# Kernel optimization log

Hardware: AMD Instinct MI355X
Metric: run time of the kernel (lower is better)

The kernel has to match this reference:

```python
import jax, jax.numpy as jnp
import numpy as np

N, E, XD, H, L, G, C = 20000, 320000, 128, 256, 4, 128, 10
EPS = 1e-5


def setup_inputs() -> dict:
    key = jax.random.key(0)
    ks = jax.random.split(key, 24)
    s = 0.05
    inp = {
        "x": jax.random.normal(ks[0], (N, XD), jnp.float32),
        "edge_index": jax.random.randint(ks[1], (2, E), 0, N, jnp.int32),
        "batch": jnp.sort(jax.random.randint(ks[2], (N,), 0, G, jnp.int32)),
        "encW": jax.random.normal(ks[3], (XD, H), jnp.float32) * s,
        "encB": jnp.zeros((H,), jnp.float32),
        "convW": jax.random.normal(ks[4], (L, H, H), jnp.float32) * s,
        "convB": jnp.zeros((L, H), jnp.float32),
        "bnG": jnp.ones((L, H), jnp.float32),
        "bnB": jnp.zeros((L, H), jnp.float32),
        "fcW1": jax.random.normal(ks[5], (H, H), jnp.float32) * s,
        "fcB1": jnp.zeros((H,), jnp.float32),
        "fcG1": jnp.ones((H,), jnp.float32),
        "fcBe1": jnp.zeros((H,), jnp.float32),
        "fcW2": jax.random.normal(ks[6], (H, H), jnp.float32) * s,
        "fcB2": jnp.zeros((H,), jnp.float32),
        "fcG2": jnp.ones((H,), jnp.float32),
        "fcBe2": jnp.zeros((H,), jnp.float32),
        "fcW3": jax.random.normal(ks[7], (H, C), jnp.float32) * s,
        "fcB3": jnp.zeros((C,), jnp.float32),
    }
    return inp


def _bn(h, g, b):
    # BatchNorm1d, training-mode batch statistics (biased var), eps=1e-5
    m = h.mean(0)
    v = h.var(0)
    return g * (h - m) * jax.lax.rsqrt(v + EPS) + b


def _forward(x, edge_index, batch, encW, encB, convW, convB, bnG, bnB,
             fcW1, fcB1, fcG1, fcBe1, fcW2, fcB2, fcG2, fcBe2, fcW3, fcB3):
    src, dst = edge_index[0], edge_index[1]
    # GCN symmetric normalization with implicit self-loops (fill value 1)
    deg = jax.ops.segment_sum(jnp.ones((E,), x.dtype), dst, num_segments=N) + 1.0
    dinv = jax.lax.rsqrt(deg)
    enorm = (dinv[src] * dinv[dst])[:, None]       # [E,1]
    self_norm = (dinv * dinv)[:, None]             # [N,1] self-loop coeff

    h = x @ encW + encB                            # node encoder
    for i in range(L):
        t = h @ convW[i]                           # GCNConv linear (no bias)
        agg = jax.ops.segment_sum(t[src] * enorm, dst, num_segments=N)
        t = agg + t * self_norm + convB[i]         # aggregate + self loop + bias
        h = jax.nn.relu(_bn(t, bnG[i], bnB[i]))    # dropout is identity (eval)

    # global mean pool over graph ids
    sums = jax.ops.segment_sum(h, batch, num_segments=G)
    cnts = jax.ops.segment_sum(jnp.ones((N,), h.dtype), batch, num_segments=G)
    g = sums / jnp.maximum(cnts, 1.0)[:, None]     # [G,H]

    # fc_out: MLP(Linear->BN->ReLU->Linear) -> BN -> Linear
    m = jax.nn.relu(_bn(g @ fcW1 + fcB1, fcG1, fcBe1)) @ fcW2 + fcB2
    m = _bn(m, fcG2, fcBe2)
    return m @ fcW3 + fcB3                         # [G,C]


def reference(x, edge_index, batch, encW, encB, convW, convB, bnG, bnB,
              fcW1, fcB1, fcG1, fcBe1, fcW2, fcB2, fcG2, fcBe2, fcW3, fcB3):
    return _forward(x, edge_index, batch, encW, encB, convW, convB, bnG, bnB,
                    fcW1, fcB1, fcG1, fcBe1, fcW2, fcB2, fcG2, fcBe2, fcW3, fcB3)
```

## Files before the change

kernel.cpp:

```cpp
#include <hip/hip_runtime.h>
#include <hip/hip_bf16.h>
#include <cstddef>

#define N_NODES 20000
#define N_EDGES 320000
#define XDIM 128
#define H 256
#define LAYERS 4
#define G_GRAPHS 128
#define C_OUT 10
#define EPS_BN 1e-5f
#define NSLOT 64
#define NB 8

typedef __attribute__((ext_vector_type(8))) short short8;
typedef __attribute__((ext_vector_type(4))) float f32x4;
typedef __attribute__((address_space(3))) unsigned int lds_u32;
typedef const __attribute__((address_space(1))) unsigned int glob_u32;

__global__ void hist_kernel(const int* __restrict__ dst, int* __restrict__ cnt, int E) {
    int e = blockIdx.x * blockDim.x + threadIdx.x;
    if (e < E) atomicAdd(&cnt[dst[e]], 1);
}

__global__ void scan_kernel(const int* __restrict__ cnt, int* __restrict__ rowstart,
                            float* __restrict__ dinv, int N) {
    __shared__ int partial[1024];
    int tid = threadIdx.x;
    int chunk = (N + 1023) / 1024;
    int start = tid * chunk;
    int lsum = 0;
    for (int i = 0; i < chunk; ++i) {
        int idx = start + i;
        if (idx < N) {
            int c = cnt[idx];
            dinv[idx] = 1.0f / sqrtf((float)c + 1.0f);
            lsum += c;
        }
    }
    partial[tid] = lsum;
    __syncthreads();
    for (int off = 1; off < 1024; off <<= 1) {
        int v = (tid >= off) ? partial[tid - off] : 0;
        __syncthreads();
        partial[tid] += v;
        __syncthreads();
    }
    int run = (tid == 0) ? 0 : partial[tid - 1];
    for (int i = 0; i < chunk; ++i) {
        int idx = start + i;
        if (idx < N) { rowstart[idx] = run; run += cnt[idx]; }
    }
    if (tid == 1023) rowstart[N] = partial[1023];
}

__global__ void fill_kernel(const int* __restrict__ src, const int* __restrict__ dst,
                            const int* __restrict__ rowstart, int* __restrict__ cursor,
                            const float* __restrict__ dinv,
                            int* __restrict__ csr_src, float* __restrict__ csr_w, int E) {
    int e = blockIdx.x * blockDim.x + threadIdx.x;
    if (e < E) {
        int s = src[e], d = dst[e];
        int pos = rowstart[d] + atomicAdd(&cursor[d], 1);
        csr_src[pos] = s;
        csr_w[pos] = dinv[s] * dinv[d];
    }
}

__global__ void prep_kernel(const float* __restrict__ x, const float* __restrict__ encW,
                            const float* __restrict__ convW,
                            __hip_bfloat16* __restrict__ xbf,
                            __hip_bfloat16* __restrict__ encWT,
                            __hip_bfloat16* __restrict__ convWT) {
    int i = blockIdx.x * blockDim.x + threadIdx.x;
    const int nx = N_NODES * XDIM;
    const int ne = XDIM * H;
    const int nc = LAYERS * H * H;
    if (i < nx) {
        xbf[i] = __float2bfloat16(x[i]);
    } else if (i < nx + ne) {
        int j = i - nx;
        int r = j / H, c = j - r * H;
        encWT[c * XDIM + r] = __float2bfloat16(encW[j]);
    } else if (i < nx + ne + nc) {
        int j = i - nx - ne;
        int l = j / (H * H), rem = j - l * (H * H);
        int r = rem / H, c = rem - r * H;
        convWT[(size_t)l * H * H + c * H + r] = __float2bfloat16(convW[j]);
    }
}

__device__ __forceinline__ short bf16bits(float x) {
    __hip_bfloat16 b = __float2bfloat16(x);
    return *(short*)&b;
}

template <int K, bool FUSE_BN>
__global__ __launch_bounds__(256) void gemm_bf16_kernel(
    const void* __restrict__ Ain,
    const __hip_bfloat16* __restrict__ BT,
    const float* __restrict__ bias,
    const float* __restrict__ spart,
    const float* __restrict__ gamma,
    const float* __restrict__ beta,
    __hip_bfloat16* __restrict__ Cbf,
    int M, int Nn) {
    __shared__ short As[2][64 * 32];
    __shared__ short Bs[2][128 * 32];
    __shared__ float scs[H];
    __shared__ float shs[H];
    const short* Ash = (const short*)Ain;
    const float* Af = (const float*)Ain;
    const short* Bsh = (const short*)BT;
    int tid = threadIdx.x;
    int lane = tid & 63;
    int wave = tid >> 6;
    int quad = lane >> 4;
    int lr = lane & 15;
    int wm = (wave & 1) * 32;
    int wn = (wave >> 1) * 64;
    int Mblk = blockIdx.x * 64;
    int Nblk = blockIdx.y * 128;

    f32x4 acc[2][4];
#pragma unroll
    for (int i = 0; i < 2; ++i)
#pragma unroll
        for (int j = 0; j < 4; ++j) acc[i][j] = (f32x4){0.f, 0.f, 0.f, 0.f};

    int srow = tid >> 2, sqs = tid & 3;
    int sqg = sqs ^ ((srow >> 1) & 3);
    int arow = Mblk + srow; if (arow >= M) arow = M - 1;
    int s1 = 256 + tid;
    int brow0 = Nblk + (tid >> 2);
    int qg0 = sqg;
    int brow1 = Nblk + (s1 >> 2);
    int qg1 = (s1 & 3) ^ (((s1 >> 2) >> 1) & 3);

    if (FUSE_BN) {
        int c = tid;
        float s = 0.f, s2 = 0.f;
#pragma unroll 8
        for (int i = 0; i < NSLOT; ++i) {
            s  += spart[(size_t)i * (2 * H) + c];
            s2 += spart[(size_t)i * (2 * H) + H + c];
        }
        float invN = 1.0f / (float)N_NODES;
        float mean = s * invN;
        float var = s2 * invN - mean * mean;
        float kk = gamma[c] / sqrtf(var + EPS_BN);
        scs[c] = kk;
        shs[c] = beta[c] - mean * kk;
        __syncthreads();
    }

    float4 ra0, ra1;
    auto loadA_f = [&](int k0) {
        int kc = k0 + sqg * 8;
        ra0 = *(const float4*)(Af + (size_t)arow * K + kc);
        ra1 = *(const float4*)(Af + (size_t)arow * K + kc + 4);
    };
    auto storeA_f = [&](int buf, int k0) {
        int kc = k0 + sqg * 8;
        float4 c0 = *(const float4*)&scs[kc];
        float4 c1 = *(const float4*)&scs[kc + 4];
        float4 h0 = *(const float4*)&shs[kc];
        float4 h1 = *(const float4*)&shs[kc + 4];
        short8 pk;
        pk[0] = bf16bits(fmaxf(ra0.x * c0.x + h0.x, 0.f));
        pk[1] = bf16bits(fmaxf(ra0.y * c0.y + h0.y, 0.f));
        pk[2] = bf16bits(fmaxf(ra0.z * c0.z + h0.z, 0.f));
        pk[3] = bf16bits(fmaxf(ra0.w * c0.w + h0.w, 0.f));
        pk[4] = bf16bits(fmaxf(ra1.x * c1.x + h1.x, 0.f));
        pk[5] = bf16bits(fmaxf(ra1.y * c1.y + h1.y, 0.f));
        pk[6] = bf16bits(fmaxf(ra1.z * c1.z + h1.z, 0.f));
        pk[7] = bf16bits(fmaxf(ra1.w * c1.w + h1.w, 0.f));
        *(short8*)&As[buf][srow * 32 + sqs * 8] = pk;
    };
    auto stageA_async = [&](int buf, int k0) {
        __builtin_amdgcn_global_load_lds((glob_u32*)(Ash + (size_t)arow * K + k0 + sqg * 8),
                                         (lds_u32*)&As[buf][0] + wave * 256, 16, 0, 0);
    };
    auto stageB = [&](int buf, int k0) {
        __builtin_amdgcn_global_load_lds((glob_u32*)(Bsh + (size_t)brow0 * K + k0 + qg0 * 8),
                                         (lds_u32*)&Bs[buf][0] + wave * 256, 16, 0, 0);
        __builtin_amdgcn_global_load_lds((glob_u32*)(Bsh + (size_t)brow1 * K + k0 + qg1 * 8),
                                         (lds_u32*)&Bs[buf][0] + 1024 + wave * 256, 16, 0, 0);
    };

    constexpr int NK = K / 32;
    if (FUSE_BN) loadA_f(0); else stageA_async(0, 0);
    stageB(0, 0);
#pragma unroll
    for (int k = 0; k < NK; ++k) {
        int buf = k & 1;
        if (FUSE_BN) storeA_f(buf, k * 32);
        __syncthreads();
        if (k + 1 < NK) {
            if (FUSE_BN) loadA_f((k + 1) * 32); else stageA_async(buf ^ 1, (k + 1) * 32);
            stageB(buf ^ 1, (k + 1) * 32);
        }
        short8 af[2], bfr[4];
#pragma unroll
        for (int mi = 0; mi < 2; ++mi) {
            int r = wm + mi * 16 + lr;
            af[mi] = *(const short8*)&As[buf][r * 32 + (quad ^ ((r >> 1) & 3)) * 8];
        }
#pragma unroll
        for (int ni = 0; ni < 4; ++ni) {
            int r = wn + ni * 16 + lr;
            bfr[ni] = *(const short8*)&Bs[buf][r * 32 + (quad ^ ((r >> 1) & 3)) * 8];
        }
#pragma unroll
        for (int mi = 0; mi < 2; ++mi)
#pragma unroll
            for (int ni = 0; ni < 4; ++ni)
                acc[mi][ni] = __builtin_amdgcn_mfma_f32_16x16x32_bf16(af[mi], bfr[ni], acc[mi][ni], 0, 0, 0);
    }
#pragma unroll
    for (int mi = 0; mi < 2; ++mi) {
#pragma unroll
        for (int r = 0; r < 4; ++r) {
            int m = Mblk + wm + mi * 16 + quad * 4 + r;
            if (m < M) {
#pragma unroll
                for (int ni = 0; ni < 4; ++ni) {
                    int n = Nblk + wn + ni * 16 + lr;
                    float v = acc[mi][ni][r];
                    if (bias) v += bias[n];
                    Cbf[(size_t)m * Nn + n] = __float2bfloat16(v);
                }
            }
        }
    }
}

__global__ __launch_bounds__(256) void agg_kernel(const __hip_bfloat16* __restrict__ t,
                           const int* __restrict__ rowstart,
                           const int* __restrict__ csr_src,
                           const float* __restrict__ csr_w,
                           const float* __restrict__ dinv,
                           const float* __restrict__ convB,
                           float* __restrict__ out,
                           float* __restrict__ spart,
                           int N) {
    __shared__ float red[2][4][256];
    int tid = threadIdx.x;
    int wave = tid >> 6;
    int lane = tid & 63;
    int sub = lane >> 5;
    int hl = lane & 31;
    int stream = wave * 2 + sub;
    int c0 = hl * 8;
    const ushort* tp = (const ushort*)t;
    float sv = 0.f, sq = 0.f;
    int n0 = blockIdx.x * NB;
#pragma unroll 1
    for (int it = 0; it < NB; ++it) {
        int n = n0 + it;
        int s = rowstart[n], e = rowstart[n + 1];
        float a[8] = {};
#pragma unroll 1
        for (int j0 = s; j0 < e; j0 += 16) {
#pragma unroll
            for (int u = 0; u < 2; ++u) {
                int j = j0 + u * 8 + stream;
                int idx = n; float w = 0.f;
                if (j < e) { idx = csr_src[j]; w = csr_w[j]; }
                uint4 v = *(const uint4*)(tp + (size_t)idx * H + c0);
                a[0] += __uint_as_float(v.x << 16) * w;
                a[1] += __uint_as_float(v.x & 0xffff0000u) * w;
                a[2] += __uint_as_float(v.y << 16) * w;
                a[3] += __uint_as_float(v.y & 0xffff0000u) * w;
                a[4] += __uint_as_float(v.z << 16) * w;
                a[5] += __uint_as_float(v.z & 0xffff0000u) * w;
                a[6] += __uint_as_float(v.w << 16) * w;
                a[7] += __uint_as_float(v.w & 0xffff0000u) * w;
            }
        }
#pragma unroll
        for (int k = 0; k < 8; ++k) a[k] += __shfl_xor(a[k], 32);
        int buf = it & 1;
        if (sub == 0) {
            *(float4*)&red[buf][wave][c0] = make_float4(a[0], a[1], a[2], a[3]);
            *(float4*)&red[buf][wave][c0 + 4] = make_float4(a[4], a[5], a[6], a[7]);
        }
        __syncthreads();
        int c = tid;
        float val = red[buf][0][c] + red[buf][1][c] + red[buf][2][c] + red[buf][3][c];
        float dn = dinv[n];
        val += __bfloat162float(t[(size_t)n * H + c]) * (dn * dn) + convB[c];
        out[(size_t)n * H + c] = val;
        sv += val; sq += val * val;
    }
    float* sp = spart + (size_t)(blockIdx.x & (NSLOT - 1)) * (2 * H);
    atomicAdd(&sp[tid], sv);
    atomicAdd(&sp[H + tid], sq);
}

__global__ __launch_bounds__(256) void pool_kernel(const float* __restrict__ t2,
                            const int* __restrict__ batch,
                            const float* __restrict__ spart,
                            const float* __restrict__ gamma,
                            const float* __restrict__ beta,
                            float* __restrict__ g, int N) {
    __shared__ float4 red[4][64];
    __shared__ float scs[H];
    __shared__ float shs[H];
    {
        int c = threadIdx.x;
        float s = 0.f, s2 = 0.f;
#pragma unroll 8
        for (int i = 0; i < NSLOT; ++i) {
            s  += spart[(size_t)i * (2 * H) + c];
            s2 += spart[(size_t)i * (2 * H) + H + c];
        }
        float invN = 1.0f / (float)N_NODES;
        float mean = s * invN;
        float var = s2 * invN - mean * mean;
        float kk = gamma[c] / sqrtf(var + EPS_BN);
        scs[c] = kk;
        shs[c] = beta[c] - mean * kk;
    }
    __syncthreads();
    int gid = blockIdx.x;
    int lo = 0, hi = N;
    while (lo < hi) { int mid = (lo + hi) >> 1; if (batch[mid] < gid) lo = mid + 1; else hi = mid; }
    int s = lo;
    lo = s; hi = N;
    while (lo < hi) { int mid = (lo + hi) >> 1; if (batch[mid] < gid + 1) lo = mid + 1; else hi = mid; }
    int e = lo;
    int wave = threadIdx.x >> 6;
    int lane = threadIdx.x & 63;
    float4 scv = *(const float4*)&scs[lane * 4];
    float4 shv = *(const float4*)&shs[lane * 4];
    float a0 = 0.f, a1 = 0.f, a2 = 0.f, a3 = 0.f;
    for (int r = s + wave; r < e; r += 4) {
        float4 v = *(const float4*)(t2 + (size_t)r * H + lane * 4);
        a0 += __bfloat162float(__float2bfloat16(fmaxf(v.x * scv.x + shv.x, 0.f)));
        a1 += __bfloat162float(__float2bfloat16(fmaxf(v.y * scv.y + shv.y, 0.f)));
        a2 += __bfloat162float(__float2bfloat16(fmaxf(v.z * scv.z + shv.z, 0.f)));
        a3 += __bfloat162float(__float2bfloat16(fmaxf(v.w * scv.w + shv.w, 0.f)));
    }
    red[wave][lane] = make_float4(a0, a1, a2, a3);
    __syncthreads();
    int c = threadIdx.x;
    const float* rf = (const float*)red;
    float sum = rf[c] + rf[256 + c] + rf[512 + c] + rf[768 + c];
    g[(size_t)gid * H + c] = sum / fmaxf((float)(e - s), 1.0f);
}

template <int K, int NN>
__global__ __launch_bounds__(256) void fc_lds_kernel(const float* __restrict__ in,
                                                     const float* __restrict__ W,
                                                     const float* __restrict__ b,
                                                     float* __restrict__ out) {
    __shared__ float row[K];
    int g = blockIdx.x;
    for (int k = threadIdx.x; k < K; k += 256) row[k] = in[(size_t)g * K + k];
    __syncthreads();
    int hc = threadIdx.x;
    if (hc < NN) {
        float acc = b[hc];
#pragma unroll
        for (int k = 0; k < K; ++k) acc += row[k] * W[k * NN + hc];
        out[(size_t)g * NN + hc] = acc;
    }
}

__global__ void fc_out_kernel(const float* __restrict__ in, const float* __restrict__ W,
                              const float* __restrict__ b, float* __restrict__ out) {
    int t = blockIdx.x * blockDim.x + threadIdx.x;
    if (t >= G_GRAPHS * C_OUT) return;
    int g = t / C_OUT, c = t % C_OUT;
    float acc = b[c];
#pragma unroll 16
    for (int k = 0; k < H; ++k) acc += in[(size_t)g * H + k] * W[k * C_OUT + c];
    out[t] = acc;
}

__global__ void bn_head_kernel(const float* __restrict__ in, const float* __restrict__ gamma,
                               const float* __restrict__ beta, float* __restrict__ out,
                               int Grows, int relu) {
    int c = blockIdx.x;
    int r = threadIdx.x;
    __shared__ float red[G_GRAPHS];
    float v = in[r * H + c];
    red[r] = v;
    __syncthreads();
    for (int off = G_GRAPHS / 2; off > 0; off >>= 1) {
        if (r < off) red[r] += red[r + off];
        __syncthreads();
    }
    float mean = red[0] / (float)Grows;
    __syncthreads();
    float d = v - mean;
    red[r] = d * d;
    __syncthreads();
    for (int off = G_GRAPHS / 2; off > 0; off >>= 1) {
        if (r < off) red[r] += red[r + off];
        __syncthreads();
    }
    float var = red[0] / (float)Grows;
    float y = gamma[c] * d / sqrtf(var + EPS_BN) + beta[c];
    if (relu) y = fmaxf(y, 0.f);
    out[r * H + c] = y;
}

extern "C" void kernel_launch(void* const* d_in, const int* in_sizes, int n_in,
                              void* d_out, int out_size, void* d_ws, size_t ws_size,
                              hipStream_t stream) {
    const float* x     = (const float*)d_in[0];
    const int*   edge  = (const int*)d_in[1];
    const int*   batch = (const int*)d_in[2];
    const float* encW  = (const float*)d_in[3];
    const float* encB  = (const float*)d_in[4];
    const float* convW = (const float*)d_in[5];
    const float* convB = (const float*)d_in[6];
    const float* bnG   = (const float*)d_in[7];
    const float* bnB   = (const float*)d_in[8];
    const float* fcW1  = (const float*)d_in[9];
    const float* fcB1  = (const float*)d_in[10];
    const float* fcG1  = (const float*)d_in[11];
    const float* fcBe1 = (const float*)d_in[12];
    const float* fcW2  = (const float*)d_in[13];
    const float* fcB2  = (const float*)d_in[14];
    const float* fcG2  = (const float*)d_in[15];
    const float* fcBe2 = (const float*)d_in[16];
    const float* fcW3  = (const float*)d_in[17];
    const float* fcB3  = (const float*)d_in[18];
    float* out = (float*)d_out;

    const int* srcIdx = edge;
    const int* dstIdx = edge + N_EDGES;

    char* base = (char*)d_ws;
    size_t off = 0;
    auto alloc = [&](size_t bytes) -> void* {
        void* p = base + off;
        off = (off + bytes + 255) & ~(size_t)255;
        return p;
    };
    int*   cnt      = (int*)alloc(N_NODES * 4);
    int*   cursor   = (int*)alloc(N_NODES * 4);
    int*   rowstart = (int*)alloc((N_NODES + 1) * 4);
    float* dinv     = (float*)alloc(N_NODES * 4);
    int*   csr_src  = (int*)alloc(N_EDGES * 4);
    float* csr_w    = (float*)alloc(N_EDGES * 4);
    float* spart    = (float*)alloc((size_t)LAYERS * NSLOT * 2 * H * 4);
    __hip_bfloat16* xbf    = (__hip_bfloat16*)alloc((size_t)N_NODES * XDIM * 2);
    __hip_bfloat16* encWT  = (__hip_bfloat16*)alloc((size_t)H * XDIM * 2);
    __hip_bfloat16* convWT = (__hip_bfloat16*)alloc((size_t)LAYERS * H * H * 2);
    __hip_bfloat16* hbf    = (__hip_bfloat16*)alloc((size_t)N_NODES * H * 2);
    __hip_bfloat16* tbf    = (__hip_bfloat16*)alloc((size_t)N_NODES * H * 2);
    float* t2buf = (float*)alloc((size_t)N_NODES * H * 4);
    float* gpool = (float*)alloc(G_GRAPHS * H * 4);
    float* m1    = (float*)alloc(G_GRAPHS * H * 4);
    float* m2    = (float*)alloc(G_GRAPHS * H * 4);

    hipMemsetAsync(cnt, 0, (size_t)((char*)rowstart - (char*)cnt), stream);
    hipMemsetAsync(spart, 0, (size_t)LAYERS * NSLOT * 2 * H * 4, stream);

    hist_kernel<<<(N_EDGES + 255) / 256, 256, 0, stream>>>(dstIdx, cnt, N_EDGES);
    scan_kernel<<<1, 1024, 0, stream>>>(cnt, rowstart, dinv, N_NODES);
    fill_kernel<<<(N_EDGES + 255) / 256, 256, 0, stream>>>(srcIdx, dstIdx, rowstart, cursor,
                                                           dinv, csr_src, csr_w, N_EDGES);

    {
        int total = N_NODES * XDIM + XDIM * H + LAYERS * H * H;
        prep_kernel<<<(total + 255) / 256, 256, 0, stream>>>(x, encW, convW, xbf, encWT, convWT);
    }

    dim3 gridG((N_NODES + 63) / 64, H / 128);
    gemm_bf16_kernel<XDIM, false><<<gridG, 256, 0, stream>>>(
        xbf, encWT, encB, nullptr, nullptr, nullptr, hbf, N_NODES, H);

    for (int l = 0; l < LAYERS; ++l) {
        float* spartL = spart + (size_t)l * NSLOT * 2 * H;
        if (l == 0) {
            gemm_bf16_kernel<H, false><<<gridG, 256, 0, stream>>>(
                hbf, convWT + (size_t)l * H * H, nullptr, nullptr, nullptr, nullptr,
                tbf, N_NODES, H);
        } else {
            float* spartP = spart + (size_t)(l - 1) * NSLOT * 2 * H;
            gemm_bf16_kernel<H, true><<<gridG, 256, 0, stream>>>(
                t2buf, convWT + (size_t)l * H * H, nullptr,
                spartP, bnG + (size_t)(l - 1) * H, bnB + (size_t)(l - 1) * H,
                tbf, N_NODES, H);
        }
        agg_kernel<<<N_NODES / NB, 256, 0, stream>>>(tbf, rowstart, csr_src, csr_w, dinv,
                                                     convB + l * H, t2buf, spartL, N_NODES);
    }

    pool_kernel<<<G_GRAPHS, 256, 0, stream>>>(
        t2buf, batch, spart + (size_t)(LAYERS - 1) * NSLOT * 2 * H,
        bnG + (size_t)(LAYERS - 1) * H, bnB + (size_t)(LAYERS - 1) * H, gpool, N_NODES);

    fc_lds_kernel<H, H><<<G_GRAPHS, 256, 0, stream>>>(gpool, fcW1, fcB1, m1);
    bn_head_kernel<<<H, G_GRAPHS, 0, stream>>>(m1, fcG1, fcBe1, m1, G_GRAPHS, 1);
    fc_lds_kernel<H, H><<<G_GRAPHS, 256, 0, stream>>>(m1, fcW2, fcB2, m2);
    bn_head_kernel<<<H, G_GRAPHS, 0, stream>>>(m2, fcG2, fcBe2, m2, G_GRAPHS, 0);
    fc_out_kernel<<<(G_GRAPHS * C_OUT + 255) / 256, 256, 0, stream>>>(m2, fcW3, fcB3, out);
}
```

Before: 447.0 us.

## Restructure GEMM: full-K B tile in LDS, A loaded directly to registers

The GEMM now uses a 64x64 output tile instead of 64x128, which doubles the grid along N. The whole K extent of the B (weight) tile is preloaded into LDS once, behind a single barrier. The A operand is no longer staged through LDS: each wave reads its MFMA A fragments straight from global memory into registers, with a one-step register prefetch in the fused-BN path. This removes the per-k-step barriers and LDS round trip for A. In exchange, A rows are reloaded by both N-blocks, and the larger register footprint may lower occupancy.

```diff
diff --git a/kernel.cpp b/kernel.cpp
--- a/kernel.cpp
+++ b/kernel.cpp
@@ -105,8 +105,8 @@
     const float* __restrict__ beta,
     __hip_bfloat16* __restrict__ Cbf,
     int M, int Nn) {
-    __shared__ short As[2][64 * 32];
-    __shared__ short Bs[2][128 * 32];
+    constexpr int NK = K / 32;
+    __shared__ short Bs[NK][64 * 32];
     __shared__ float scs[H];
     __shared__ float shs[H];
     const short* Ash = (const short*)Ain;
@@ -118,24 +118,19 @@
     int quad = lane >> 4;
     int lr = lane & 15;
     int wm = (wave & 1) * 32;
-    int wn = (wave >> 1) * 64;
+    int wn = (wave >> 1) * 32;
     int Mblk = blockIdx.x * 64;
-    int Nblk = blockIdx.y * 128;
-
-    f32x4 acc[2][4];
-#pragma unroll
-    for (int i = 0; i < 2; ++i)
-#pragma unroll
-        for (int j = 0; j < 4; ++j) acc[i][j] = (f32x4){0.f, 0.f, 0.f, 0.f};
+    int Nblk = blockIdx.y * 64;
 
     int srow = tid >> 2, sqs = tid & 3;
     int sqg = sqs ^ ((srow >> 1) & 3);
-    int arow = Mblk + srow; if (arow >= M) arow = M - 1;
-    int s1 = 256 + tid;
-    int brow0 = Nblk + (tid >> 2);
-    int qg0 = sqg;
-    int brow1 = Nblk + (s1 >> 2);
-    int qg1 = (s1 & 3) ^ (((s1 >> 2) >> 1) & 3);
+    int brow = Nblk + srow;
+#pragma unroll
+    for (int kc = 0; kc < NK; ++kc) {
+        __builtin_amdgcn_global_load_lds(
+            (glob_u32*)(Bsh + (size_t)brow * K + kc * 32 + sqg * 8),
+            (lds_u32*)&Bs[kc][0] + wave * 256, 16, 0, 0);
+    }
 
     if (FUSE_BN) {
         int c = tid;
@@ -151,72 +146,104 @@
         float kk = gamma[c] / sqrtf(var + EPS_BN);
         scs[c] = kk;
         shs[c] = beta[c] - mean * kk;
-        __syncthreads();
-    }
-
-    float4 ra0, ra1;
-    auto loadA_f = [&](int k0) {
-        int kc = k0 + sqg * 8;
-        ra0 = *(const float4*)(Af + (size_t)arow * K + kc);
-        ra1 = *(const float4*)(Af + (size_t)arow * K + kc + 4);
-    };
-    auto storeA_f = [&](int buf, int k0) {
-        int kc = k0 + sqg * 8;
-        float4 c0 = *(const float4*)&scs[kc];
-        float4 c1 = *(const float4*)&scs[kc + 4];
-        float4 h0 = *(const float4*)&shs[kc];
-        float4 h1 = *(const float4*)&shs[kc + 4];
-        short8 pk;
-        pk[0] = bf16bits(fmaxf(ra0.x * c0.x + h0.x, 0.f));
-        pk[1] = bf16bits(fmaxf(ra0.y * c0.y + h0.y, 0.f));
-        pk[2] = bf16bits(fmaxf(ra0.z * c0.z + h0.z, 0.f));
-        pk[3] = bf16bits(fmaxf(ra0.w * c0.w + h0.w, 0.f));
-        pk[4] = bf16bits(fmaxf(ra1.x * c1.x + h1.x, 0.f));
-        pk[5] = bf16bits(fmaxf(ra1.y * c1.y + h1.y, 0.f));
-        pk[6] = bf16bits(fmaxf(ra1.z * c1.z + h1.z, 0.f));
-        pk[7] = bf16bits(fmaxf(ra1.w * c1.w + h1.w, 0.f));
-        *(short8*)&As[buf][srow * 32 + sqs * 8] = pk;
-    };
-    auto stageA_async = [&](int buf, int k0) {
-        __builtin_amdgcn_global_load_lds((glob_u32*)(Ash + (size_t)arow * K + k0 + sqg * 8),
-                                         (lds_u32*)&As[buf][0] + wave * 256, 16, 0, 0);
-    };
-    auto stageB = [&](int buf, int k0) {
-        __builtin_amdgcn_global_load_lds((glob_u32*)(Bsh + (size_t)brow0 * K + k0 + qg0 * 8),
-                                         (lds_u32*)&Bs[buf][0] + wave * 256, 16, 0, 0);
-        __builtin_amdgcn_global_load_lds((glob_u32*)(Bsh + (size_t)brow1 * K + k0 + qg1 * 8),
-                                         (lds_u32*)&Bs[buf][0] + 1024 + wave * 256, 16, 0, 0);
-    };
-
-    constexpr int NK = K / 32;
-    if (FUSE_BN) loadA_f(0); else stageA_async(0, 0);
-    stageB(0, 0);
-#pragma unroll
-    for (int k = 0; k < NK; ++k) {
-        int buf = k & 1;
-        if (FUSE_BN) storeA_f(buf, k * 32);
-        __syncthreads();
-        if (k + 1 < NK) {
-            if (FUSE_BN) loadA_f((k + 1) * 32); else stageA_async(buf ^ 1, (k + 1) * 32);
-            stageB(buf ^ 1, (k + 1) * 32);
-        }
-        short8 af[2], bfr[4];
-#pragma unroll
-        for (int mi = 0; mi < 2; ++mi) {
-            int r = wm + mi * 16 + lr;
-            af[mi] = *(const short8*)&As[buf][r * 32 + (quad ^ ((r >> 1) & 3)) * 8];
-        }
-#pragma unroll
-        for (int ni = 0; ni < 4; ++ni) {
-            int r = wn + ni * 16 + lr;
-            bfr[ni] = *(const short8*)&Bs[buf][r * 32 + (quad ^ ((r >> 1) & 3)) * 8];
-        }
-#pragma unroll
-        for (int mi = 0; mi < 2; ++mi)
-#pragma unroll
-            for (int ni = 0; ni < 4; ++ni)
-                acc[mi][ni] = __builtin_amdgcn_mfma_f32_16x16x32_bf16(af[mi], bfr[ni], acc[mi][ni], 0, 0, 0);
-    }
+    }
+    __syncthreads();
+
+    int grow[2];
+#pragma unroll
+    for (int mi = 0; mi < 2; ++mi) {
+        int r = Mblk + wm + mi * 16 + lr;
+        grow[mi] = r < M ? r : M - 1;
+    }
+
+    f32x4 acc[2][2];
+#pragma unroll
+    for (int i = 0; i < 2; ++i)
+#pragma unroll
+        for (int j = 0; j < 2; ++j) acc[i][j] = (f32x4){0.f, 0.f, 0.f, 0.f};
+
+    if (FUSE_BN) {
+        float4 c0a, c0b, c1a, c1b;
+        {
+            int kc = 0 * 32 + quad * 8;
+            c0a = *(const float4*)(Af + (size_t)grow[0] * K + kc);
+            c0b = *(const float4*)(Af + (size_t)grow[0] * K + kc + 4);
+            c1a = *(const float4*)(Af + (size_t)grow[1] * K + kc);
+            c1b = *(const float4*)(Af + (size_t)grow[1] * K + kc + 4);
+        }
+#pragma unroll
+        for (int k = 0; k < NK; ++k) {
+            float4 n0a, n0b, n1a, n1b;
+            if (k + 1 < NK) {
+                int kc = (k + 1) * 32 + quad * 8;
+                n0a = *(const float4*)(Af + (size_t)grow[0] * K + kc);
+                n0b = *(const float4*)(Af + (size_t)grow[0] * K + kc + 4);
+                n1a = *(const float4*)(Af + (size_t)grow[1] * K + kc);
+                n1b = *(const float4*)(Af + (size_t)grow[1] * K + kc + 4);
+            }
+            int kc = k * 32 + quad * 8;
+            float4 s0 = *(const float4*)&scs[kc];
+            float4 s1 = *(const float4*)&scs[kc + 4];
+            float4 h0 = *(const float4*)&shs[kc];
+            float4 h1 = *(const float4*)&shs[kc + 4];
+            short8 aqk[2];
+            {
+                short8 pk;
+                pk[0] = bf16bits(fmaxf(c0a.x * s0.x + h0.x, 0.f));
+                pk[1] = bf16bits(fmaxf(c0a.y * s0.y + h0.y, 0.f));
+                pk[2] = bf16bits(fmaxf(c0a.z * s0.z + h0.z, 0.f));
+                pk[3] = bf16bits(fmaxf(c0a.w * s0.w + h0.w, 0.f));
+                pk[4] = bf16bits(fmaxf(c0b.x * s1.x + h1.x, 0.f));
+                pk[5] = bf16bits(fmaxf(c0b.y * s1.y + h1.y, 0.f));
+                pk[6] = bf16bits(fmaxf(c0b.z * s1.z + h1.z, 0.f));
+                pk[7] = bf16bits(fmaxf(c0b.w * s1.w + h1.w, 0.f));
+                aqk[0] = pk;
+                pk[0] = bf16bits(fmaxf(c1a.x * s0.x + h0.x, 0.f));
+                pk[1] = bf16bits(fmaxf(c1a.y * s0.y + h0.y, 0.f));
+                pk[2] = bf16bits(fmaxf(c1a.z * s0.z + h0.z, 0.f));
+                pk[3] = bf16bits(fmaxf(c1a.w * s0.w + h0.w, 0.f));
+                pk[4] = bf16bits(fmaxf(c1b.x * s1.x + h1.x, 0.f));
+                pk[5] = bf16bits(fmaxf(c1b.y * s1.y + h1.y, 0.f));
+                pk[6] = bf16bits(fmaxf(c1b.z * s1.z + h1.z, 0.f));
+                pk[7] = bf16bits(fmaxf(c1b.w * s1.w + h1.w, 0.f));
+                aqk[1] = pk;
+            }
+            short8 bfr[2];
+#pragma unroll
+            for (int ni = 0; ni < 2; ++ni) {
+                int r = wn + ni * 16 + lr;
+                bfr[ni] = *(const short8*)&Bs[k][r * 32 + (quad ^ ((r >> 1) & 3)) * 8];
+            }
+#pragma unroll
+            for (int mi = 0; mi < 2; ++mi)
+#pragma unroll
+                for (int ni = 0; ni < 2; ++ni)
+                    acc[mi][ni] = __builtin_amdgcn_mfma_f32_16x16x32_bf16(aqk[mi], bfr[ni], acc[mi][ni], 0, 0, 0);
+            c0a = n0a; c0b = n0b; c1a = n1a; c1b = n1b;
+        }
+    } else {
+        short8 aq[NK][2];
+#pragma unroll
+        for (int k = 0; k < NK; ++k)
+#pragma unroll
+            for (int mi = 0; mi < 2; ++mi)
+                aq[k][mi] = *(const short8*)(Ash + (size_t)grow[mi] * K + k * 32 + quad * 8);
+#pragma unroll
+        for (int k = 0; k < NK; ++k) {
+            short8 bfr[2];
+#pragma unroll
+            for (int ni = 0; ni < 2; ++ni) {
+                int r = wn + ni * 16 + lr;
+                bfr[ni] = *(const short8*)&Bs[k][r * 32 + (quad ^ ((r >> 1) & 3)) * 8];
+            }
+#pragma unroll
+            for (int mi = 0; mi < 2; ++mi)
+#pragma unroll
+                for (int ni = 0; ni < 2; ++ni)
+                    acc[mi][ni] = __builtin_amdgcn_mfma_f32_16x16x32_bf16(aq[k][mi], bfr[ni], acc[mi][ni], 0, 0, 0);
+        }
+    }
+
 #pragma unroll
     for (int mi = 0; mi < 2; ++mi) {
 #pragma unroll
@@ -224,7 +251,7 @@
             int m = Mblk + wm + mi * 16 + quad * 4 + r;
             if (m < M) {
 #pragma unroll
-                for (int ni = 0; ni < 4; ++ni) {
+                for (int ni = 0; ni < 2; ++ni) {
                     int n = Nblk + wn + ni * 16 + lr;
                     float v = acc[mi][ni][r];
                     if (bias) v += bias[n];
@@ -471,7 +498,7 @@
         prep_kernel<<<(total + 255) / 256, 256, 0, stream>>>(x, encW, convW, xbf, encWT, convWT);
     }
 
-    dim3 gridG((N_NODES + 63) / 64, H / 128);
+    dim3 gridG((N_NODES + 63) / 64, H / 64);
     gemm_bf16_kernel<XDIM, false><<<gridG, 256, 0, stream>>>(
         xbf, encWT, encB, nullptr, nullptr, nullptr, hbf, N_NODES, H);
 
```

Result: slower. 490.2 us (+9.7%).
